# Kernel tuning notes

Measured on AMD Instinct MI355X. Metric: run time of the kernel, lower is better.

## Reference

```python
import jax, jax.numpy as jnp
import numpy as np

B, N, E = 8, 2048, 1024


def setup_inputs() -> dict:
    key = jax.random.key(0)
    x = jax.random.normal(key, (B, N, E), dtype=jnp.float32)
    pos = jnp.ones((N - 1,), dtype=jnp.float32)
    zero = jnp.ones((1,), dtype=jnp.float32)
    neg = jnp.ones((N - 1,), dtype=jnp.float32)
    return {"x": x, "pos": pos, "zero": zero, "neg": neg}


def reference(x, pos, zero, neg):
    # x: [b, n, e]; Toeplitz matvec via circular FFT convolution of length 2n.
    b, n, e = x.shape
    # circulant kernel: [zero, pos[:n-1], zero, neg[-(n-1):]] -> length 2n
    a = jnp.concatenate([zero, pos[: n - 1], zero, neg[-(n - 1):]])
    # torch: fft(x, 2n, dim=1, norm='ortho')
    y = jnp.fft.fft(x, n=2 * n, axis=1, norm="ortho")  # [b, 2n, e] complex
    # torch: fft(a) with default ('backward') norm, i.e. unnormalized forward
    v = jnp.fft.fft(a)[None, :, None]                   # [1, 2n, 1]
    u = v * y
    out = jnp.fft.ifft(u, n=2 * n, axis=1, norm="ortho")[:, :n, :].real
    return out.astype(x.dtype)
```

## Files before the change

### kernel.cpp

```cpp
#include <hip/hip_runtime.h>
#include <stdint.h>


#define B_ 8
#define N_ 2048
#define NF 4096
#define E_ 1024

__device__ __forceinline__ int P(int n) {
    return n ^ ((n >> 4) & 15) ^ ((n >> 8) & 15) ^ (((n >> 9) & 1) << 4);
}
#define PERM(r) ((((r) & 3) << 2) | ((r) >> 2))

__device__ __forceinline__ unsigned short f32_to_bf16_rne(float f) {
    union { float f; unsigned int u; } cv; cv.f = f;
    unsigned int u = cv.u;
    u += 0x7fffu + ((u >> 16) & 1u);
    return (unsigned short)(u >> 16);
}
__device__ __forceinline__ float bf16_to_f32(unsigned short u) {
    union { unsigned int u; float f; } cv; cv.u = ((unsigned int)u) << 16; return cv.f;
}
__device__ __forceinline__ uint32_t cpack(float re, float im) {
    union { float f; uint32_t u; } a, b; a.f = re; b.f = im;
    uint32_t ua = a.u + (0x7fffu + ((a.u >> 16) & 1u));
    uint32_t ub = b.u + (0x7fffu + ((b.u >> 16) & 1u));
    return __builtin_amdgcn_perm(ub, ua, 0x07060302u);
}
__device__ __forceinline__ void cunpack(uint32_t u, float& re, float& im) {
    union { uint32_t u; float f; } a, b;
    a.u = u << 16; b.u = u & 0xffff0000u;
    re = a.f; im = b.f;
}
__device__ __forceinline__ void cmul(float& ar, float& ai, float br, float bi) {
    float t = ar * br - ai * bi; ai = ar * bi + ai * br; ar = t;
}
__device__ __forceinline__ void cmulc(float& ar, float& ai, float br, float bi) {
    float t = ar * br + ai * bi; ai = ai * br - ar * bi; ar = t;
}

__device__ __forceinline__ void dft4(float& x0r, float& x0i, float& x1r, float& x1i,
                                     float& x2r, float& x2i, float& x3r, float& x3i,
                                     float sg) {
    float t0r = x0r + x2r, t0i = x0i + x2i;
    float t1r = x0r - x2r, t1i = x0i - x2i;
    float t2r = x1r + x3r, t2i = x1i + x3i;
    float t3r = x1r - x3r, t3i = x1i - x3i;
    x0r = t0r + t2r; x0i = t0i + t2i;
    x2r = t0r - t2r; x2i = t0i - t2i;
    x1r = t1r - sg * t3i; x1i = t1i + sg * t3r;
    x3r = t1r + sg * t3i; x3i = t1i - sg * t3r;
}

template<int SG>
__device__ __forceinline__ void dft16_layer1(float* xr, float* xi) {
    const float sg = (float)SG;
#pragma unroll
    for (int n0 = 0; n0 < 4; ++n0)
        dft4(xr[n0], xi[n0], xr[n0 + 4], xi[n0 + 4],
             xr[n0 + 8], xi[n0 + 8], xr[n0 + 12], xi[n0 + 12], sg);
}
template<int SG>
__device__ __forceinline__ void dft16_layer1_pad(float* xr, float* xi) {
    const float sg = (float)SG;
#pragma unroll
    for (int n0 = 0; n0 < 4; ++n0) {
        float ar = xr[n0], ai = xi[n0], br = xr[n0 + 4], bi = xi[n0 + 4];
        xr[n0]      = ar + br;       xi[n0]      = ai + bi;
        xr[n0 + 4]  = ar - sg * bi;  xi[n0 + 4]  = ai + sg * br;
        xr[n0 + 8]  = ar - br;       xi[n0 + 8]  = ai - bi;
        xr[n0 + 12] = ar + sg * bi;  xi[n0 + 12] = ai - sg * br;
    }
}
template<int SG>
__device__ __forceinline__ void dft16_twiddle(float* xr, float* xi) {
    const float sg = (float)SG;
    const float C1 = 0.923879532511286756f;
    const float S1 = 0.382683432365089772f;
    const float H  = 0.707106781186547524f;
    cmul(xr[5],  xi[5],  C1,  sg * S1);
    cmul(xr[9],  xi[9],  H,   sg * H);
    cmul(xr[13], xi[13], S1,  sg * C1);
    cmul(xr[6],  xi[6],  H,   sg * H);
    cmul(xr[10], xi[10], 0.f, sg);
    cmul(xr[14], xi[14], -H,  sg * H);
    cmul(xr[7],  xi[7],  S1,  sg * C1);
    cmul(xr[11], xi[11], -H,  sg * H);
    cmul(xr[15], xi[15], -C1, -sg * S1);
}
template<int SG>
__device__ __forceinline__ void dft16_layer2(float* xr, float* xi) {
    const float sg = (float)SG;
#pragma unroll
    for (int k1 = 0; k1 < 4; ++k1)
        dft4(xr[4 * k1], xi[4 * k1], xr[4 * k1 + 1], xi[4 * k1 + 1],
             xr[4 * k1 + 2], xi[4 * k1 + 2], xr[4 * k1 + 3], xi[4 * k1 + 3], sg);
}
template<int SG>
__device__ __forceinline__ void dft16(float* xr, float* xi) {
    dft16_layer1<SG>(xr, xi);
    dft16_twiddle<SG>(xr, xi);
    dft16_layer2<SG>(xr, xi);
}

template<int L>
__device__ __forceinline__ void fwd_stage_sincos(float2* buf, int t) {
    constexpr int Lq = L / 16;
    int g = t / Lq;
    int j = t - g * Lq;
    int base = g * L + j;
    const float TPI = -6.28318530717958647692f;
    float xr[16], xi[16];
#pragma unroll
    for (int r = 0; r < 16; ++r) {
        float2 v = buf[P(base + r * Lq)];
        xr[r] = v.x; xi[r] = v.y;
    }
    dft16<-1>(xr, xi);
    { float2 v; v.x = xr[0]; v.y = xi[0]; buf[P(base)] = v; }
#pragma unroll
    for (int r = 1; r < 16; ++r) {
        float s, c;
        __sincosf(TPI * (float)(j * r) * (1.f / (float)L), &s, &c);
        float yr = xr[PERM(r)], yi = xi[PERM(r)];
        cmul(yr, yi, c, s);
        float2 v; v.x = yr; v.y = yi;
        buf[P(base + r * Lq)] = v;
    }
}

__global__ __launch_bounds__(256) void prep(const float* __restrict__ x,
                                            const float* __restrict__ pos,
                                            const float* __restrict__ zero,
                                            const float* __restrict__ neg,
                                            uint32_t* __restrict__ xP,
                                            float2* __restrict__ tw4096,
                                            float2* __restrict__ tw256,
                                            float2* __restrict__ V2) {
    __shared__ __align__(16) char smraw[32768];
    const float TPI = -6.28318530717958647692f;
    int blk = blockIdx.x, t = threadIdx.x;
    if (blk < 16) {
        float s, c;
        __sincosf(TPI * (float)(blk * t) * (1.f / 4096.f), &s, &c);
        float2 v; v.x = c; v.y = s;
        tw4096[blk * 256 + t] = v;
    } else if (blk == 16) {
        int r = t >> 4, j = t & 15;
        float s, c;
        __sincosf(TPI * (float)(r * j) * (1.f / 256.f), &s, &c);
        float2 v; v.x = c; v.y = s;
        tw256[t] = v;
    } else if (blk == 17) {
        float2* buf = (float2*)smraw;
#pragma unroll
        for (int it = 0; it < 16; ++it) {
            int n = t + 256 * it;
            float v;
            if (n == 0) v = zero[0];
            else if (n < N_) v = pos[n - 1];
            else if (n == N_) v = zero[0];
            else v = neg[n - (N_ + 1)];
            float2 cc; cc.x = v; cc.y = 0.f;
            buf[P(n)] = cc;
        }
        __syncthreads();
        fwd_stage_sincos<4096>(buf, t); __syncthreads();
        fwd_stage_sincos<256>(buf, t);  __syncthreads();
        fwd_stage_sincos<16>(buf, t);   __syncthreads();
        const float s = 1.f / (float)NF;
#pragma unroll
        for (int it = 0; it < 16; ++it) {
            int n = t + 256 * it;
            float2 c = buf[P(n)];
            c.x *= s; c.y *= s;
            V2[n] = c;
        }
    } else {
        float (*tile)[66] = (float (*)[66])smraw;
        int tid = blk - 18;
        int e0 = (tid & 15) * 64;
        int j0 = ((tid >> 4) & 31) * 64;
        int b  = tid >> 9;
        int e4 = t & 15, jr = t >> 4;
#pragma unroll
        for (int it = 0; it < 4; ++it) {
            int j = jr + it * 16;
            const float4 v = *(const float4*)(x + ((size_t)(b * N_ + j0 + j) * E_) + e0 + e4 * 4);
            tile[e4 * 4 + 0][j] = v.x;
            tile[e4 * 4 + 1][j] = v.y;
            tile[e4 * 4 + 2][j] = v.z;
            tile[e4 * 4 + 3][j] = v.w;
        }
        __syncthreads();
        int jj = t & 63, ur = t >> 6;
#pragma unroll
        for (int it = 0; it < 8; ++it) {
            int u = ur + it * 4;
            union { unsigned short s[2]; uint32_t w; } pk;
            pk.s[0] = f32_to_bf16_rne(tile[2 * u][jj]);
            pk.s[1] = f32_to_bf16_rne(tile[2 * u + 1][jj]);
            xP[((size_t)(b * 512 + (e0 >> 1) + u)) * N_ + j0 + jj] = pk.w;
        }
    }
}

__global__ __launch_bounds__(256) void fft_conv(const uint32_t* __restrict__ xP,
                                                const float2* __restrict__ tw4096,
                                                const float2* __restrict__ tw256,
                                                const float2* __restrict__ V2,
                                                float* __restrict__ out) {
    __shared__ uint32_t buf0[NF];
    __shared__ uint32_t buf1[NF];
    int t = threadIdx.x;
    int bid = blockIdx.x;
    int xcd = bid & 7;
    int q = bid >> 3;
    int b = q >> 5;
    int quad = xcd * 32 + (q & 31);
    const uint32_t* g0 = xP + ((size_t)(b * 512 + quad * 2)) * N_;
    const uint32_t* g1 = g0 + N_;

    float x0r[16], x0i[16], x1r[16], x1i[16];

#pragma unroll
    for (int r = 0; r < 8; ++r) {
        int n = t + 256 * r;
        cunpack(g0[n], x0r[r], x0i[r]);
        cunpack(g1[n], x1r[r], x1i[r]);
    }
#pragma unroll
    for (int r = 8; r < 16; ++r) { x0r[r] = 0.f; x0i[r] = 0.f; x1r[r] = 0.f; x1i[r] = 0.f; }
    dft16_layer1_pad<-1>(x0r, x0i); dft16_layer1_pad<-1>(x1r, x1i);
    dft16_twiddle<-1>(x0r, x0i);    dft16_twiddle<-1>(x1r, x1i);
    dft16_layer2<-1>(x0r, x0i);     dft16_layer2<-1>(x1r, x1i);
    buf0[P(t)] = cpack(x0r[0], x0i[0]);
    buf1[P(t)] = cpack(x1r[0], x1i[0]);
#pragma unroll
    for (int r = 1; r < 16; ++r) {
        float2 w = tw4096[r * 256 + t];
        int a = P(t + 256 * r);
        float y0r = x0r[PERM(r)], y0i = x0i[PERM(r)];
        cmul(y0r, y0i, w.x, w.y);
        buf0[a] = cpack(y0r, y0i);
        float y1r = x1r[PERM(r)], y1i = x1i[PERM(r)];
        cmul(y1r, y1i, w.x, w.y);
        buf1[a] = cpack(y1r, y1i);
    }
    __syncthreads();

    int g = t >> 4, j = t & 15;
    int base = g * 256 + j;
#pragma unroll
    for (int r = 0; r < 16; ++r) {
        int a = P(base + 16 * r);
        cunpack(buf0[a], x0r[r], x0i[r]);
        cunpack(buf1[a], x1r[r], x1i[r]);
    }
    dft16<-1>(x0r, x0i); dft16<-1>(x1r, x1i);
    buf0[P(base)] = cpack(x0r[0], x0i[0]);
    buf1[P(base)] = cpack(x1r[0], x1i[0]);
#pragma unroll
    for (int r = 1; r < 16; ++r) {
        float2 w = tw256[r * 16 + j];
        int a = P(base + 16 * r);
        float y0r = x0r[PERM(r)], y0i = x0i[PERM(r)];
        cmul(y0r, y0i, w.x, w.y);
        buf0[a] = cpack(y0r, y0i);
        float y1r = x1r[PERM(r)], y1i = x1i[PERM(r)];
        cmul(y1r, y1i, w.x, w.y);
        buf1[a] = cpack(y1r, y1i);
    }
    __syncthreads();

    {
        int mb = 16 * t;
#pragma unroll
        for (int r = 0; r < 16; ++r) {
            int a = P(mb + r);
            cunpack(buf0[a], x0r[r], x0i[r]);
            cunpack(buf1[a], x1r[r], x1i[r]);
        }
        dft16<-1>(x0r, x0i); dft16<-1>(x1r, x1i);
#pragma unroll
        for (int r = 0; r < 16; ++r) {
            int p = PERM(r);
            if (p < r) continue;
            if (p == r) {
                float2 vv = V2[mb + r];
                float ar = x0r[r], ai = x0i[r];
                x0r[r] = ar * vv.x - ai * vv.y; x0i[r] = ar * vv.y + ai * vv.x;
                ar = x1r[r]; ai = x1i[r];
                x1r[r] = ar * vv.x - ai * vv.y; x1i[r] = ar * vv.y + ai * vv.x;
            } else {
                float2 va = V2[mb + r], vb = V2[mb + p];
                float ar = x0r[r], ai = x0i[r], br = x0r[p], bi = x0i[p];
                x0r[r] = br * va.x - bi * va.y; x0i[r] = br * va.y + bi * va.x;
                x0r[p] = ar * vb.x - ai * vb.y; x0i[p] = ar * vb.y + ai * vb.x;
                ar = x1r[r]; ai = x1i[r]; br = x1r[p]; bi = x1i[p];
                x1r[r] = br * va.x - bi * va.y; x1i[r] = br * va.y + bi * va.x;
                x1r[p] = ar * vb.x - ai * vb.y; x1i[p] = ar * vb.y + ai * vb.x;
            }
        }
        dft16<1>(x0r, x0i); dft16<1>(x1r, x1i);
#pragma unroll
        for (int r = 0; r < 16; ++r) {
            int a = P(mb + r);
            buf0[a] = cpack(x0r[PERM(r)], x0i[PERM(r)]);
            buf1[a] = cpack(x1r[PERM(r)], x1i[PERM(r)]);
        }
    }
    __syncthreads();

#pragma unroll
    for (int r = 0; r < 16; ++r) {
        int a = P(base + 16 * r);
        cunpack(buf0[a], x0r[r], x0i[r]);
        cunpack(buf1[a], x1r[r], x1i[r]);
    }
#pragma unroll
    for (int r = 1; r < 16; ++r) {
        float2 w = tw256[r * 16 + j];
        cmulc(x0r[r], x0i[r], w.x, w.y);
        cmulc(x1r[r], x1i[r], w.x, w.y);
    }
    dft16<1>(x0r, x0i); dft16<1>(x1r, x1i);
#pragma unroll
    for (int r = 0; r < 16; ++r) {
        int a = P(base + 16 * r);
        buf0[a] = cpack(x0r[PERM(r)], x0i[PERM(r)]);
        buf1[a] = cpack(x1r[PERM(r)], x1i[PERM(r)]);
    }
    __syncthreads();

#pragma unroll
    for (int r = 0; r < 16; ++r) {
        int a = P(t + 256 * r);
        cunpack(buf0[a], x0r[r], x0i[r]);
        cunpack(buf1[a], x1r[r], x1i[r]);
    }
#pragma unroll
    for (int r = 1; r < 16; ++r) {
        float2 w = tw4096[r * 256 + t];
        cmulc(x0r[r], x0i[r], w.x, w.y);
        cmulc(x1r[r], x1i[r], w.x, w.y);
    }
    dft16_layer1<1>(x0r, x0i); dft16_layer1<1>(x1r, x1i);
    dft16_twiddle<1>(x0r, x0i); dft16_twiddle<1>(x1r, x1i);
    float* ob = out + ((size_t)b * N_) * E_ + quad * 4;
#pragma unroll
    for (int k1 = 0; k1 < 4; ++k1) {
        float a0r = x0r[4 * k1],     a0i = x0i[4 * k1];
        float a1r = x0r[4 * k1 + 1], a1i = x0i[4 * k1 + 1];
        float a2r = x0r[4 * k1 + 2], a2i = x0i[4 * k1 + 2];
        float a3r = x0r[4 * k1 + 3], a3i = x0i[4 * k1 + 3];
        float t0r = a0r + a2r, t0i = a0i + a2i;
        float t1r = a0r - a2r, t1i = a0i - a2i;
        float t2r = a1r + a3r, t2i = a1i + a3i;
        float t3r = a1r - a3r, t3i = a1i - a3i;
        float s0v0r = t0r + t2r, s0v0i = t0i + t2i;
        float s0v1r = t1r - t3i, s0v1i = t1i + t3r;
        a0r = x1r[4 * k1];     a0i = x1i[4 * k1];
        a1r = x1r[4 * k1 + 1]; a1i = x1i[4 * k1 + 1];
        a2r = x1r[4 * k1 + 2]; a2i = x1i[4 * k1 + 2];
        a3r = x1r[4 * k1 + 3]; a3i = x1i[4 * k1 + 3];
        t0r = a0r + a2r; t0i = a0i + a2i;
        t1r = a0r - a2r; t1i = a0i - a2i;
        t2r = a1r + a3r; t2i = a1i + a3i;
        t3r = a1r - a3r; t3i = a1i - a3i;
        float s1v0r = t0r + t2r, s1v0i = t0i + t2i;
        float s1v1r = t1r - t3i, s1v1i = t1i + t3r;
        float4 w0; w0.x = s0v0r; w0.y = s0v0i; w0.z = s1v0r; w0.w = s1v0i;
        float4 w1; w1.x = s0v1r; w1.y = s0v1i; w1.z = s1v1r; w1.w = s1v1i;
        *(float4*)(ob + (size_t)(t + 256 * k1) * E_)       = w0;
        *(float4*)(ob + (size_t)(t + 256 * (k1 + 4)) * E_) = w1;
    }
}

__global__ __launch_bounds__(256) void naive_toep(const float* __restrict__ x,
                                                  const float* __restrict__ pos,
                                                  const float* __restrict__ zero,
                                                  const float* __restrict__ neg,
                                                  float* __restrict__ out) {
    int bid = blockIdx.x;
    int e   = (bid & 3) * 256 + threadIdx.x;
    int k   = (bid >> 2) & (N_ - 1);
    int b   = bid >> 13;
    float zv = zero[0];
    float acc = 0.f;
    const float* xb = x + (size_t)b * N_ * E_ + e;
    for (int jj = 0; jj < N_; ++jj) {
        float c = (jj < k) ? pos[k - jj - 1] : (jj == k) ? zv : neg[N_ - 1 - jj + k];
        acc += c * xb[(size_t)jj * E_];
    }
    out[((size_t)(b * N_ + k)) * E_ + e] = acc;
}

extern "C" void kernel_launch(void* const* d_in, const int* in_sizes, int n_in,
                              void* d_out, int out_size, void* d_ws, size_t ws_size,
                              hipStream_t stream) {
    const float* x    = (const float*)d_in[0];
    const float* pos  = (const float*)d_in[1];
    const float* zero = (const float*)d_in[2];
    const float* neg  = (const float*)d_in[3];
    float* out = (float*)d_out;

    const size_t needX = (size_t)B_ * 512 * N_ * sizeof(uint32_t);
    const size_t need  = needX + (2 * (size_t)NF + 256) * sizeof(float2);
    if (ws_size >= need) {
        uint32_t* xP   = (uint32_t*)d_ws;
        float2* tw4096 = (float2*)((char*)d_ws + needX);
        float2* tw256  = tw4096 + NF;
        float2* V2     = tw256 + 256;
        prep<<<18 + 4096, 256, 0, stream>>>(x, pos, zero, neg, xP, tw4096, tw256, V2);
        fft_conv<<<2048, 256, 0, stream>>>(xP, tw4096, tw256, V2, out);
    } else {
        naive_toep<<<65536, 256, 0, stream>>>(x, pos, zero, neg, out);
    }
}
```

Baseline: 174.5 us.

## Read fp32 input directly in FFT kernel, drop bf16 transpose pre-pass

Removes the prep-kernel transpose that packed x into a bf16, sequence-major buffer. The FFT kernel now loads float4 strided rows straight from x, four embedding columns per block, and treats them as two complex signals. This saves a full read and write of x plus the extra workspace, but the loads are now strided by E per thread (16 bytes per row). It also keeps fp32 input precision in the first FFT layer.

```diff
diff --git a/kernel.cpp b/kernel.cpp
--- a/kernel.cpp
+++ b/kernel.cpp
@@ -12,15 +12,6 @@
 }
 #define PERM(r) ((((r) & 3) << 2) | ((r) >> 2))
 
-__device__ __forceinline__ unsigned short f32_to_bf16_rne(float f) {
-    union { float f; unsigned int u; } cv; cv.f = f;
-    unsigned int u = cv.u;
-    u += 0x7fffu + ((u >> 16) & 1u);
-    return (unsigned short)(u >> 16);
-}
-__device__ __forceinline__ float bf16_to_f32(unsigned short u) {
-    union { unsigned int u; float f; } cv; cv.u = ((unsigned int)u) << 16; return cv.f;
-}
 __device__ __forceinline__ uint32_t cpack(float re, float im) {
     union { float f; uint32_t u; } a, b; a.f = re; b.f = im;
     uint32_t ua = a.u + (0x7fffu + ((a.u >> 16) & 1u));
@@ -129,11 +120,9 @@
     }
 }
 
-__global__ __launch_bounds__(256) void prep(const float* __restrict__ x,
-                                            const float* __restrict__ pos,
+__global__ __launch_bounds__(256) void prep(const float* __restrict__ pos,
                                             const float* __restrict__ zero,
                                             const float* __restrict__ neg,
-                                            uint32_t* __restrict__ xP,
                                             float2* __restrict__ tw4096,
                                             float2* __restrict__ tw256,
                                             float2* __restrict__ V2) {
@@ -151,7 +140,7 @@
         __sincosf(TPI * (float)(r * j) * (1.f / 256.f), &s, &c);
         float2 v; v.x = c; v.y = s;
         tw256[t] = v;
-    } else if (blk == 17) {
+    } else {
         float2* buf = (float2*)smraw;
 #pragma unroll
         for (int it = 0; it < 16; ++it) {
@@ -176,36 +165,10 @@
             c.x *= s; c.y *= s;
             V2[n] = c;
         }
-    } else {
-        float (*tile)[66] = (float (*)[66])smraw;
-        int tid = blk - 18;
-        int e0 = (tid & 15) * 64;
-        int j0 = ((tid >> 4) & 31) * 64;
-        int b  = tid >> 9;
-        int e4 = t & 15, jr = t >> 4;
-#pragma unroll
-        for (int it = 0; it < 4; ++it) {
-            int j = jr + it * 16;
-            const float4 v = *(const float4*)(x + ((size_t)(b * N_ + j0 + j) * E_) + e0 + e4 * 4);
-            tile[e4 * 4 + 0][j] = v.x;
-            tile[e4 * 4 + 1][j] = v.y;
-            tile[e4 * 4 + 2][j] = v.z;
-            tile[e4 * 4 + 3][j] = v.w;
-        }
-        __syncthreads();
-        int jj = t & 63, ur = t >> 6;
-#pragma unroll
-        for (int it = 0; it < 8; ++it) {
-            int u = ur + it * 4;
-            union { unsigned short s[2]; uint32_t w; } pk;
-            pk.s[0] = f32_to_bf16_rne(tile[2 * u][jj]);
-            pk.s[1] = f32_to_bf16_rne(tile[2 * u + 1][jj]);
-            xP[((size_t)(b * 512 + (e0 >> 1) + u)) * N_ + j0 + jj] = pk.w;
-        }
-    }
-}
-
-__global__ __launch_bounds__(256) void fft_conv(const uint32_t* __restrict__ xP,
+    }
+}
+
+__global__ __launch_bounds__(256) void fft_conv(const float* __restrict__ x,
                                                 const float2* __restrict__ tw4096,
                                                 const float2* __restrict__ tw256,
                                                 const float2* __restrict__ V2,
@@ -218,16 +181,15 @@
     int q = bid >> 3;
     int b = q >> 5;
     int quad = xcd * 32 + (q & 31);
-    const uint32_t* g0 = xP + ((size_t)(b * 512 + quad * 2)) * N_;
-    const uint32_t* g1 = g0 + N_;
 
     float x0r[16], x0i[16], x1r[16], x1i[16];
 
+    const float* gx = x + ((size_t)b * N_) * E_ + (size_t)quad * 4;
 #pragma unroll
     for (int r = 0; r < 8; ++r) {
-        int n = t + 256 * r;
-        cunpack(g0[n], x0r[r], x0i[r]);
-        cunpack(g1[n], x1r[r], x1i[r]);
+        const float4 v = *(const float4*)(gx + (size_t)(t + 256 * r) * E_);
+        x0r[r] = v.x; x0i[r] = v.y;
+        x1r[r] = v.z; x1i[r] = v.w;
     }
 #pragma unroll
     for (int r = 8; r < 16; ++r) { x0r[r] = 0.f; x0i[r] = 0.f; x1r[r] = 0.f; x1i[r] = 0.f; }
@@ -405,15 +367,13 @@
     const float* neg  = (const float*)d_in[3];
     float* out = (float*)d_out;
 
-    const size_t needX = (size_t)B_ * 512 * N_ * sizeof(uint32_t);
-    const size_t need  = needX + (2 * (size_t)NF + 256) * sizeof(float2);
+    const size_t need = (2 * (size_t)NF + 256) * sizeof(float2);
     if (ws_size >= need) {
-        uint32_t* xP   = (uint32_t*)d_ws;
-        float2* tw4096 = (float2*)((char*)d_ws + needX);
+        float2* tw4096 = (float2*)d_ws;
         float2* tw256  = tw4096 + NF;
         float2* V2     = tw256 + 256;
-        prep<<<18 + 4096, 256, 0, stream>>>(x, pos, zero, neg, xP, tw4096, tw256, V2);
-        fft_conv<<<2048, 256, 0, stream>>>(xP, tw4096, tw256, V2, out);
+        prep<<<18, 256, 0, stream>>>(pos, zero, neg, tw4096, tw256, V2);
+        fft_conv<<<2048, 256, 0, stream>>>(x, tw4096, tw256, V2, out);
     } else {
         naive_toep<<<65536, 256, 0, stream>>>(x, pos, zero, neg, out);
     }
```

Result: slower. 186.7 us (+7.0%).
